# Optimization experiments

Measured on AMD Instinct MI355X. Metric: run time of the kernel, lower is better.

Reference implementation:

```python
import jax, jax.numpy as jnp
import numpy as np

NUM_HEADS = 8  # init num_heads


def setup_inputs() -> dict:
    key = jax.random.key(0)
    ks = jax.random.split(key, 8)
    B, N, C, G = 2, 256 * 256, 256, 512  # N hardcoded by original reshape(256*256)
    xq = jax.random.normal(ks[0], (B, N, C), jnp.float32)
    xk = jax.random.normal(ks[1], (B, N, C), jnp.float32)
    xv = jax.random.normal(ks[2], (B, N, C), jnp.float32)
    w_scale = C ** -0.5
    Wq = jax.random.normal(ks[3], (C, C), jnp.float32) * w_scale
    bq = jax.random.normal(ks[4], (C,), jnp.float32) * 0.02
    Wp = jax.random.normal(ks[5], (C, C), jnp.float32) * w_scale
    bp = jax.random.normal(ks[6], (C,), jnp.float32) * 0.02
    # Voronoi cell labels 1..G, each cell exactly N//G tokens, randomly scattered
    # over the 256x256 grid (irregular gather/scatter access, all cells < 1500 tokens).
    labels = jnp.repeat(jnp.arange(1, G + 1, dtype=jnp.int32), N // G)
    Voronoi = jnp.stack([
        jax.random.permutation(jax.random.fold_in(ks[7], b), labels) for b in range(B)
    ]).reshape(B, 256, 256)
    return {"xq": xq, "xk": xk, "xv": xv, "Wq": Wq, "bq": bq,
            "Wp": Wp, "bp": bp, "Voronoi": Voronoi, "num_groups": G}


def reference(xq, xk, xv, Wq, bq, Wp, bp, Voronoi, num_groups):
    B, N, C = xq.shape
    H = NUM_HEADS
    hd = C // H
    scale = hd ** -0.5  # qk_scale default: head_dim ** -0.5
    # NOTE: the original forward projects q, k AND v with self.q (shared weights/bias).
    # This (likely a bug upstream) is preserved faithfully here.
    q = (xq @ Wq.T + bq).reshape(B, N, H, hd)
    k = (xk @ Wq.T + bq).reshape(B, N, H, hd)
    v = (xv @ Wq.T + bq).reshape(B, N, H, hd)
    labels = Voronoi.reshape(B, N)
    order = jnp.argsort(labels, axis=1)   # [B, N] sort tokens by Voronoi cell id
    inv = jnp.argsort(order, axis=1)      # inverse permutation for scatter-back
    S = N // num_groups                   # tokens per cell (static)

    def gather(t):  # [B, N, H, hd] -> [B, G, S, H, hd] grouped by cell
        return jnp.take_along_axis(t, order[:, :, None, None], axis=1).reshape(B, num_groups, S, H, hd)

    qg = gather(q) * scale
    kg = gather(k)
    vg = gather(v)
    attn = jnp.einsum('bgshd,bgthd->bghst', qg, kg)   # per-cell scores [B,G,H,S,S]
    p = jax.nn.softmax(attn, axis=-1)                 # attn_drop=0 (eval)
    og = jnp.einsum('bghst,bgthd->bgshd', p, vg).reshape(B, N, H, hd)
    out = jnp.take_along_axis(og, inv[:, :, None, None], axis=1).reshape(B, N, C)
    return out @ Wp.T + bp                            # proj_drop=0 (eval)
```

## Files before the change

### kernel.cpp

```cpp
#include <hip/hip_runtime.h>
#include <hip/hip_bf16.h>

#define B_    2
#define NTOK  65536
#define C_    256
#define H_    8
#define HD_   32
#define G_    512
#define S_    128
#define BN    (B_*NTOK)
#define M3    (3*BN)

typedef __attribute__((ext_vector_type(8))) short short8;
typedef __attribute__((ext_vector_type(4))) float f32x4;

__device__ __forceinline__ ushort f2bf(float f) {
  __bf16 h = (__bf16)f;
  return __builtin_bit_cast(unsigned short, h);
}
__device__ __forceinline__ unsigned pk2(float lo, float hi) {
  return (unsigned)f2bf(lo) | ((unsigned)f2bf(hi) << 16);
}

__device__ __forceinline__ void gl16(const void* g, void* l) {
  __builtin_amdgcn_global_load_lds(
      (const __attribute__((address_space(1))) unsigned int*)g,
      (__attribute__((address_space(3))) unsigned int*)l, 16, 0, 0);
}

#define SW4(c, r) ((((c) ^ (r) ^ ((r) >> 2))) & 3)
#define SWK32(c, r) ((((c) ^ ((r) >> 1))) & 3)
#define VSL(c, ch) ((((c) ^ (((ch) & 7) << 1) ^ (((ch) >> 3) & 3))) & 15)

#define QSCALE 0.25506907131737264f

__global__ __launch_bounds__(256) void k_prep(const float* __restrict__ Wq,
                                              const float* __restrict__ Wp,
                                              ushort* __restrict__ Wq_img,
                                              ushort* __restrict__ Wp_img) {
  int gid = blockIdx.x * 256 + threadIdx.x;
  int w = gid >> 13, rem = gid & 8191;
  if (w == 0) {
    int ks = rem >> 11, rem2 = rem & 2047;
    int r = rem2 >> 3, c = rem2 & 7;
    const float4* s = reinterpret_cast<const float4*>(Wq + (size_t)r * 256 + ks * 64 + c * 8);
    float4 a = s[0], b = s[1];
    uint4 o;
    o.x = pk2(a.x, a.y); o.y = pk2(a.z, a.w);
    o.z = pk2(b.x, b.y); o.w = pk2(b.z, b.w);
    *reinterpret_cast<uint4*>(Wq_img + ks * 16384 + r * 64 + ((c ^ (r & 7)) << 3)) = o;
  } else {
    int h = rem >> 10, r = (rem >> 2) & 255, c = rem & 3;
    const float4* s = reinterpret_cast<const float4*>(Wp + (size_t)r * 256 + h * 32 + c * 8);
    float4 a = s[0], b = s[1];
    uint4 o;
    o.x = pk2(a.x, a.y); o.y = pk2(a.z, a.w);
    o.z = pk2(b.x, b.y); o.w = pk2(b.z, b.w);
    *reinterpret_cast<uint4*>(Wp_img + h * 8192 + r * 32 + (SWK32(c, r) << 3)) = o;
  }
}

__global__ __launch_bounds__(256) void k_group(const int* __restrict__ vor,
                                               int* __restrict__ grp,
                                               int* __restrict__ cnt) {
  int idx = blockIdx.x * 256 + threadIdx.x;
  int b = idx >> 16;
  int n = idx & (NTOK - 1);
  int g = vor[idx] - 1;
  int pos = atomicAdd(&cnt[(b << 9) + g], 1);
  grp[((b << 9) + g) * S_ + pos] = n;
}

__global__ __launch_bounds__(512, 4) void k_proj_qkv(
    const float* __restrict__ xq, const float* __restrict__ xk,
    const float* __restrict__ xv, const ushort* __restrict__ Wq_img,
    const float* __restrict__ bq, ushort* __restrict__ qkv) {
  __shared__ ushort As[128 * 64];
  __shared__ ushort Bs[2][256 * 64];
  int mt = blockIdx.x;
  int t = mt >> 10;
  const float* A = (t == 0) ? xq : (t == 1) ? xk : xv;
  float qsc = (t == 0) ? QSCALE : 1.0f;
  size_t abase = (size_t)(mt & 1023) * 128 * 256;
  int row0 = mt * 128;

  int tid = threadIdx.x, lane = tid & 63, wave = tid >> 6;
  int l15 = lane & 15, hi = lane >> 4;
  int wr = (wave >> 2) * 64, wc = (wave & 3) * 64;
  int sr = tid >> 2, sq = tid & 3;

  const float* aptr = A + abase + (size_t)sr * 256 + sq * 16;
  int boff = wave * 4096 + lane * 16;

  f32x4 acc[4][4] = {};
  float4 ar[2][4];
  {
    const float4* p = reinterpret_cast<const float4*>(aptr);
#pragma unroll
    for (int j = 0; j < 4; ++j) ar[0][j] = p[j];
  }
#pragma unroll
  for (int j = 0; j < 4; ++j)
    gl16((const char*)Wq_img + boff + j * 1024, (char*)Bs[0] + boff + j * 1024);

#pragma unroll
  for (int ks = 0; ks < 4; ++ks) {
    uint4 w0, w1;
    w0.x = pk2(ar[ks & 1][0].x, ar[ks & 1][0].y); w0.y = pk2(ar[ks & 1][0].z, ar[ks & 1][0].w);
    w0.z = pk2(ar[ks & 1][1].x, ar[ks & 1][1].y); w0.w = pk2(ar[ks & 1][1].z, ar[ks & 1][1].w);
    w1.x = pk2(ar[ks & 1][2].x, ar[ks & 1][2].y); w1.y = pk2(ar[ks & 1][2].z, ar[ks & 1][2].w);
    w1.z = pk2(ar[ks & 1][3].x, ar[ks & 1][3].y); w1.w = pk2(ar[ks & 1][3].z, ar[ks & 1][3].w);
    *reinterpret_cast<uint4*>(&As[sr * 64 + (((sq * 2) ^ (sr & 7)) << 3)]) = w0;
    *reinterpret_cast<uint4*>(&As[sr * 64 + (((sq * 2 + 1) ^ (sr & 7)) << 3)]) = w1;
    if (ks < 3) {
      const float4* p = reinterpret_cast<const float4*>(aptr + (ks + 1) * 64);
#pragma unroll
      for (int j = 0; j < 4; ++j) ar[(ks + 1) & 1][j] = p[j];
#pragma unroll
      for (int j = 0; j < 4; ++j)
        gl16((const char*)Wq_img + (ks + 1) * 32768 + boff + j * 1024,
             (char*)Bs[(ks + 1) & 1] + boff + j * 1024);
      asm volatile("s_waitcnt vmcnt(8)" ::: "memory");
    } else {
      asm volatile("s_waitcnt vmcnt(0)" ::: "memory");
    }
    asm volatile("s_waitcnt lgkmcnt(0)" ::: "memory");
    __builtin_amdgcn_s_barrier();
    const ushort* Bcur = Bs[ks & 1];
#pragma unroll
    for (int kk = 0; kk < 2; ++kk) {
      int ck = kk * 4 + hi;
      short8 af[4], bfr[4];
#pragma unroll
      for (int m = 0; m < 4; ++m) {
        int r = wr + m * 16 + l15;
        af[m] = *reinterpret_cast<const short8*>(&As[r * 64 + ((ck ^ (r & 7)) << 3)]);
      }
#pragma unroll
      for (int n = 0; n < 4; ++n) {
        int r = wc + n * 16 + l15;
        bfr[n] = *reinterpret_cast<const short8*>(&Bcur[r * 64 + ((ck ^ (r & 7)) << 3)]);
      }
#pragma unroll
      for (int m = 0; m < 4; ++m)
#pragma unroll
        for (int n = 0; n < 4; ++n)
          acc[m][n] = __builtin_amdgcn_mfma_f32_16x16x32_bf16(af[m], bfr[n], acc[m][n], 0, 0, 0);
    }
    asm volatile("s_waitcnt lgkmcnt(0)" ::: "memory");
    __builtin_amdgcn_s_barrier();
  }

  ushort* Ot = (ushort*)Bs;
#pragma unroll
  for (int n = 0; n < 4; ++n) {
    int col = wc + n * 16 + l15;
    float bv = bq[col];
    int c = col >> 3, ci = col & 7;
#pragma unroll
    for (int m = 0; m < 4; ++m) {
      int r0 = wr + m * 16 + hi * 4;
#pragma unroll
      for (int j = 0; j < 4; ++j) {
        int r = r0 + j;
        int slot = c ^ (((r >> 2) & 3) << 1);
        Ot[r * 256 + slot * 8 + ci] = f2bf((acc[m][n][j] + bv) * qsc);
      }
    }
  }
  __syncthreads();
  {
    size_t gbase = (size_t)row0 * 256;
#pragma unroll
    for (int s = 0; s < 8; ++s) {
      int off = s * 4096 + tid * 8;
      int r = off >> 8, cc = (off >> 3) & 31;
      int slot = cc ^ (((r >> 2) & 3) << 1);
      *reinterpret_cast<uint4*>(qkv + gbase + off) =
          *reinterpret_cast<const uint4*>(Ot + r * 256 + slot * 8);
    }
  }
}

__global__ __launch_bounds__(512) void k_attn_proj(
    const ushort* __restrict__ qkv, const int* __restrict__ grp,
    const ushort* __restrict__ Wp_img, const float* __restrict__ bp,
    float* __restrict__ out) {
  __shared__ int toks[128];
  __shared__ ushort shm[32768];
  ushort* Qs  = shm;
  ushort* Ks  = shm + 4096;
  ushort* Vt  = shm + 8192;
  ushort* Oh  = shm + 12288;
  ushort* Wp0 = shm + 16384;
  ushort* Wp1 = shm + 24576;

  int bid = blockIdx.x;
  int g = bid & (G_ - 1), b = bid >> 9;
  int tid = threadIdx.x, lane = tid & 63, wave = tid >> 6;
  int l15 = lane & 15, hi = lane >> 4;
  int strip = wave * 16;
  int mg = wave >> 1, ng = wave & 1;

  if (tid < 128) toks[tid] = grp[((b << 9) + g) * S_ + tid];
  __syncthreads();

  int wpoff = wave * 1024 + lane * 16;
  gl16((const char*)Wp_img + wpoff, (char*)Wp0 + wpoff);
  gl16((const char*)Wp_img + 8192 + wpoff, (char*)Wp0 + wpoff + 8192);

  f32x4 acc[2][8] = {};

  int r_st = tid >> 2, cp = tid & 3;
  int tok_st = toks[r_st];
  size_t rowq = (size_t)(b * NTOK + tok_st) * 256;
  int chunk_t = r_st >> 3, tl = r_st & 7;

  uint4 qa, ka, va;
  {
    size_t base = rowq + cp * 8;
    qa = *reinterpret_cast<const uint4*>(qkv + base);
    ka = *reinterpret_cast<const uint4*>(qkv + (size_t)BN * 256 + base);
    va = *reinterpret_cast<const uint4*>(qkv + (size_t)2 * BN * 256 + base);
  }

  for (int h = 0; h < 8; ++h) {
    ushort* WpCur = (h & 1) ? Wp1 : Wp0;
    ushort* WpNext = (h & 1) ? Wp0 : Wp1;
    *reinterpret_cast<uint4*>(&Qs[r_st * 32 + SW4(cp, r_st) * 8]) = qa;
    *reinterpret_cast<uint4*>(&Ks[r_st * 32 + SW4(cp, r_st) * 8]) = ka;
    {
      const ushort* pv_ = reinterpret_cast<const ushort*>(&va);
#pragma unroll
      for (int e = 0; e < 8; ++e) {
        int ch = cp * 8 + e;
        Vt[ch * 128 + (VSL(chunk_t, ch) << 3) + tl] = pv_[e];
      }
    }
    asm volatile("s_waitcnt lgkmcnt(0)" ::: "memory");
    __builtin_amdgcn_s_barrier();

    if (h < 7) {
      gl16((const char*)Wp_img + (h + 1) * 16384 + wpoff, (char*)WpNext + wpoff);
      gl16((const char*)Wp_img + (h + 1) * 16384 + 8192 + wpoff, (char*)WpNext + wpoff + 8192);
      size_t base = rowq + (h + 1) * 32 + cp * 8;
      qa = *reinterpret_cast<const uint4*>(qkv + base);
      ka = *reinterpret_cast<const uint4*>(qkv + (size_t)BN * 256 + base);
      va = *reinterpret_cast<const uint4*>(qkv + (size_t)2 * BN * 256 + base);
    }

    f32x4 sacc[8] = {};
    {
      int ra = strip + l15;
      short8 qf = *reinterpret_cast<const short8*>(&Qs[ra * 32 + SW4(hi, ra) * 8]);
      __builtin_amdgcn_s_setprio(1);
#pragma unroll
      for (int n = 0; n < 8; ++n) {
        int r = n * 16 + l15;
        short8 kf = *reinterpret_cast<const short8*>(&Ks[r * 32 + SW4(hi, r) * 8]);
        sacc[n] = __builtin_amdgcn_mfma_f32_16x16x32_bf16(kf, qf, sacc[n], 0, 0, 0);
      }
      __builtin_amdgcn_s_setprio(0);
    }

    float mx = -1e30f;
#pragma unroll
    for (int n = 0; n < 8; ++n)
#pragma unroll
      for (int j = 0; j < 4; ++j) mx = fmaxf(mx, sacc[n][j]);
    mx = fmaxf(mx, __shfl_xor(mx, 16));
    mx = fmaxf(mx, __shfl_xor(mx, 32));
    float p[8][4];
    float sum = 0.f;
#pragma unroll
    for (int n = 0; n < 8; ++n)
#pragma unroll
      for (int j = 0; j < 4; ++j) { p[n][j] = exp2f(sacc[n][j] - mx); sum += p[n][j]; }
    sum += __shfl_xor(sum, 16);
    sum += __shfl_xor(sum, 32);
    float inv = 1.0f / sum;

    short8 paf[4];
#pragma unroll
    for (int t = 0; t < 4; ++t) {
      unsigned e0 = pk2(p[2 * t][0], p[2 * t][1]);
      unsigned e1 = pk2(p[2 * t][2], p[2 * t][3]);
      unsigned o0 = pk2(p[2 * t + 1][0], p[2 * t + 1][1]);
      unsigned o1 = pk2(p[2 * t + 1][2], p[2 * t + 1][3]);
      unsigned pe0 = __shfl_xor(e0, 16), pe1 = __shfl_xor(e1, 16);
      unsigned po0 = __shfl_xor(o0, 16), po1 = __shfl_xor(o1, 16);
      bool up = (hi & 1);
      unsigned E0 = up ? pe0 : e0, E1 = up ? pe1 : e1;
      unsigned E2 = up ? e0 : pe0, E3 = up ? e1 : pe1;
      unsigned O0 = up ? po0 : o0, O1 = up ? po1 : o1;
      unsigned O2 = up ? o0 : po0, O3 = up ? o1 : po1;
      unsigned s0 = up ? E0 : O0, s1 = up ? E1 : O1;
      unsigned s2 = up ? E2 : O2, s3 = up ? E3 : O3;
      unsigned r0 = __shfl_xor(s0, 32), r1 = __shfl_xor(s1, 32);
      unsigned r2 = __shfl_xor(s2, 32), r3 = __shfl_xor(s3, 32);
      unsigned f0, f1, f2, f3;
      if (hi == 0)      { f0 = E0; f1 = E1; f2 = E2; f3 = E3; }
      else if (hi == 3) { f0 = O0; f1 = O1; f2 = O2; f3 = O3; }
      else              { f0 = r0; f1 = r1; f2 = r2; f3 = r3; }
      union { unsigned u[4]; short8 s; } cv;
      cv.u[0] = f0; cv.u[1] = f1; cv.u[2] = f2; cv.u[3] = f3;
      paf[t] = cv.s;
    }

    f32x4 oacc[2] = {};
    __builtin_amdgcn_s_setprio(1);
#pragma unroll
    for (int t = 0; t < 4; ++t) {
      short8 bv[2];
#pragma unroll
      for (int n2 = 0; n2 < 2; ++n2) {
        int ch = n2 * 16 + l15;
        int chunk = t * 4 + hi;
        bv[n2] = *reinterpret_cast<const short8*>(&Vt[ch * 128 + (VSL(chunk, ch) << 3)]);
      }
#pragma unroll
      for (int n2 = 0; n2 < 2; ++n2)
        oacc[n2] = __builtin_amdgcn_mfma_f32_16x16x32_bf16(paf[t], bv[n2], oacc[n2], 0, 0, 0);
    }
    __builtin_amdgcn_s_setprio(0);

    float invj[4];
#pragma unroll
    for (int jr = 0; jr < 4; ++jr) invj[jr] = __shfl(inv, hi * 4 + jr);
#pragma unroll
    for (int n2 = 0; n2 < 2; ++n2)
#pragma unroll
      for (int jr = 0; jr < 4; ++jr) {
        int row = strip + hi * 4 + jr;
        int col = n2 * 16 + l15;
        Oh[row * 32 + (SWK32(col >> 3, row) << 3) + (col & 7)] = f2bf(oacc[n2][jr] * invj[jr]);
      }
    asm volatile("s_waitcnt vmcnt(5)" ::: "memory");
    asm volatile("s_waitcnt lgkmcnt(0)" ::: "memory");
    __builtin_amdgcn_s_barrier();

    {
      short8 af[2], bf[8];
#pragma unroll
      for (int m = 0; m < 2; ++m) {
        int r = mg * 32 + m * 16 + l15;
        af[m] = *reinterpret_cast<const short8*>(&Oh[r * 32 + (SWK32(hi, r) << 3)]);
      }
#pragma unroll
      for (int n = 0; n < 8; ++n) {
        int r = ng * 128 + n * 16 + l15;
        bf[n] = *reinterpret_cast<const short8*>(&WpCur[r * 32 + (SWK32(hi, r) << 3)]);
      }
      __builtin_amdgcn_s_setprio(1);
#pragma unroll
      for (int m = 0; m < 2; ++m)
#pragma unroll
        for (int n = 0; n < 8; ++n)
          acc[m][n] = __builtin_amdgcn_mfma_f32_16x16x32_bf16(af[m], bf[n], acc[m][n], 0, 0, 0);
      __builtin_amdgcn_s_setprio(0);
    }
  }

  float* Of = (float*)shm;
#pragma unroll
  for (int q = 0; q < 4; ++q) {
    __syncthreads();
    if (mg == q) {
#pragma unroll
      for (int n = 0; n < 8; ++n) {
        int col = ng * 128 + n * 16 + l15;
        float bv = bp[col];
        int c = col >> 2, ci = col & 3;
#pragma unroll
        for (int m = 0; m < 2; ++m) {
#pragma unroll
          for (int j = 0; j < 4; ++j) {
            int lr = m * 16 + hi * 4 + j;
            int slot = c ^ (((lr >> 2) & 3) << 2);
            Of[lr * 256 + slot * 4 + ci] = acc[m][n][j] + bv;
          }
        }
      }
    }
    __syncthreads();
#pragma unroll
    for (int s = 0; s < 4; ++s) {
      int off = s * 2048 + tid * 4;
      int lr = off >> 8, cc = (off >> 2) & 63;
      int slot = cc ^ (((lr >> 2) & 3) << 2);
      int tok = toks[q * 32 + lr];
      *reinterpret_cast<float4*>(out + ((size_t)(b * NTOK + tok)) * 256 + cc * 4) =
          *reinterpret_cast<const float4*>(Of + lr * 256 + slot * 4);
    }
  }
}

extern "C" void kernel_launch(void* const* d_in, const int* in_sizes, int n_in,
                              void* d_out, int out_size, void* d_ws, size_t ws_size,
                              hipStream_t stream) {
  const float* xq = (const float*)d_in[0];
  const float* xk = (const float*)d_in[1];
  const float* xv = (const float*)d_in[2];
  const float* Wq = (const float*)d_in[3];
  const float* bq = (const float*)d_in[4];
  const float* Wp = (const float*)d_in[5];
  const float* bp = (const float*)d_in[6];
  const int*   vor = (const int*)d_in[7];

  char* ws = (char*)d_ws;
  ushort* qkv    = (ushort*)ws;
  int*    grp    = (int*)(ws + (size_t)201326592);
  int*    cnt    = (int*)(ws + (size_t)201850880);
  ushort* Wq_img = (ushort*)(ws + (size_t)201854976);
  ushort* Wp_img = (ushort*)(ws + (size_t)201986048);

  hipMemsetAsync(cnt, 0, B_ * G_ * sizeof(int), stream);
  k_prep<<<dim3(64), dim3(256), 0, stream>>>(Wq, Wp, Wq_img, Wp_img);
  k_group<<<dim3(BN / 256), dim3(256), 0, stream>>>(vor, grp, cnt);
  k_proj_qkv<<<dim3(M3 / 128), dim3(512), 0, stream>>>(xq, xk, xv, Wq_img, bq, qkv);
  k_attn_proj<<<dim3(B_ * G_), dim3(512), 0, stream>>>(qkv, grp, Wp_img, bp, (float*)d_out);
}
```

Measured before the change: 316.0 us.

## Make QKV projection persistent with full weight matrix resident in LDS

The QKV projection becomes a persistent kernel with 256 blocks. Each block loads the whole bf16 Wq image (128KB) into LDS once, and each wave then walks independent 32-row tiles over six iterations, with no block-level barriers inside the main loop. The goal is to stop re-streaming the weights per 128-row tile and to cut barrier overhead, with per-wave staging for A and for the output transpose. In exchange, the large LDS footprint limits occupancy to one block per CU, each wave does less MFMA work per A fragment (2x16 tiles), and latency hiding relies on register double-buffering of A.

```diff
diff --git a/kernel.cpp b/kernel.cpp
--- a/kernel.cpp
+++ b/kernel.cpp
@@ -41,14 +41,13 @@
   int gid = blockIdx.x * 256 + threadIdx.x;
   int w = gid >> 13, rem = gid & 8191;
   if (w == 0) {
-    int ks = rem >> 11, rem2 = rem & 2047;
-    int r = rem2 >> 3, c = rem2 & 7;
-    const float4* s = reinterpret_cast<const float4*>(Wq + (size_t)r * 256 + ks * 64 + c * 8);
+    int ks = rem >> 10, r = (rem >> 2) & 255, c = rem & 3;
+    const float4* s = reinterpret_cast<const float4*>(Wq + (size_t)r * 256 + ks * 32 + c * 8);
     float4 a = s[0], b = s[1];
     uint4 o;
     o.x = pk2(a.x, a.y); o.y = pk2(a.z, a.w);
     o.z = pk2(b.x, b.y); o.w = pk2(b.z, b.w);
-    *reinterpret_cast<uint4*>(Wq_img + ks * 16384 + r * 64 + ((c ^ (r & 7)) << 3)) = o;
+    *reinterpret_cast<uint4*>(Wq_img + ks * 8192 + r * 32 + (SWK32(c, r) << 3)) = o;
   } else {
     int h = rem >> 10, r = (rem >> 2) & 255, c = rem & 3;
     const float4* s = reinterpret_cast<const float4*>(Wp + (size_t)r * 256 + h * 32 + c * 8);
@@ -71,113 +70,113 @@
   grp[((b << 9) + g) * S_ + pos] = n;
 }
 
-__global__ __launch_bounds__(512, 4) void k_proj_qkv(
+__global__ __launch_bounds__(512, 2) void k_proj_qkv(
     const float* __restrict__ xq, const float* __restrict__ xk,
     const float* __restrict__ xv, const ushort* __restrict__ Wq_img,
     const float* __restrict__ bq, ushort* __restrict__ qkv) {
-  __shared__ ushort As[128 * 64];
-  __shared__ ushort Bs[2][256 * 64];
-  int mt = blockIdx.x;
-  int t = mt >> 10;
-  const float* A = (t == 0) ? xq : (t == 1) ? xk : xv;
-  float qsc = (t == 0) ? QSCALE : 1.0f;
-  size_t abase = (size_t)(mt & 1023) * 128 * 256;
-  int row0 = mt * 128;
-
+  __shared__ ushort Wl[65536];
+  __shared__ ushort Asl[8][1024];
   int tid = threadIdx.x, lane = tid & 63, wave = tid >> 6;
   int l15 = lane & 15, hi = lane >> 4;
-  int wr = (wave >> 2) * 64, wc = (wave & 3) * 64;
-  int sr = tid >> 2, sq = tid & 3;
-
-  const float* aptr = A + abase + (size_t)sr * 256 + sq * 16;
-  int boff = wave * 4096 + lane * 16;
-
-  f32x4 acc[4][4] = {};
+
+  {
+    int off = tid * 16;
+#pragma unroll
+    for (int s = 0; s < 16; ++s)
+      gl16((const char*)Wq_img + s * 8192 + off, (char*)Wl + s * 8192 + off);
+  }
+  asm volatile("s_waitcnt vmcnt(0)" ::: "memory");
+  __syncthreads();
+
+  ushort* As = Asl[wave];
+  int sr = lane >> 1, sc2 = (lane & 1) * 2;
+
+  float biasv[16];
+#pragma unroll
+  for (int n = 0; n < 16; ++n) biasv[n] = bq[n * 16 + l15];
+
+  int gw = blockIdx.x * 8 + wave;
+
   float4 ar[2][4];
   {
-    const float4* p = reinterpret_cast<const float4*>(aptr);
-#pragma unroll
-    for (int j = 0; j < 4; ++j) ar[0][j] = p[j];
-  }
-#pragma unroll
-  for (int j = 0; j < 4; ++j)
-    gl16((const char*)Wq_img + boff + j * 1024, (char*)Bs[0] + boff + j * 1024);
-
-#pragma unroll
-  for (int ks = 0; ks < 4; ++ks) {
-    uint4 w0, w1;
-    w0.x = pk2(ar[ks & 1][0].x, ar[ks & 1][0].y); w0.y = pk2(ar[ks & 1][0].z, ar[ks & 1][0].w);
-    w0.z = pk2(ar[ks & 1][1].x, ar[ks & 1][1].y); w0.w = pk2(ar[ks & 1][1].z, ar[ks & 1][1].w);
-    w1.x = pk2(ar[ks & 1][2].x, ar[ks & 1][2].y); w1.y = pk2(ar[ks & 1][2].z, ar[ks & 1][2].w);
-    w1.z = pk2(ar[ks & 1][3].x, ar[ks & 1][3].y); w1.w = pk2(ar[ks & 1][3].z, ar[ks & 1][3].w);
-    *reinterpret_cast<uint4*>(&As[sr * 64 + (((sq * 2) ^ (sr & 7)) << 3)]) = w0;
-    *reinterpret_cast<uint4*>(&As[sr * 64 + (((sq * 2 + 1) ^ (sr & 7)) << 3)]) = w1;
-    if (ks < 3) {
-      const float4* p = reinterpret_cast<const float4*>(aptr + (ks + 1) * 64);
-#pragma unroll
-      for (int j = 0; j < 4; ++j) ar[(ks + 1) & 1][j] = p[j];
-#pragma unroll
-      for (int j = 0; j < 4; ++j)
-        gl16((const char*)Wq_img + (ks + 1) * 32768 + boff + j * 1024,
-             (char*)Bs[(ks + 1) & 1] + boff + j * 1024);
-      asm volatile("s_waitcnt vmcnt(8)" ::: "memory");
-    } else {
-      asm volatile("s_waitcnt vmcnt(0)" ::: "memory");
-    }
-    asm volatile("s_waitcnt lgkmcnt(0)" ::: "memory");
-    __builtin_amdgcn_s_barrier();
-    const ushort* Bcur = Bs[ks & 1];
-#pragma unroll
-    for (int kk = 0; kk < 2; ++kk) {
-      int ck = kk * 4 + hi;
-      short8 af[4], bfr[4];
-#pragma unroll
-      for (int m = 0; m < 4; ++m) {
-        int r = wr + m * 16 + l15;
-        af[m] = *reinterpret_cast<const short8*>(&As[r * 64 + ((ck ^ (r & 7)) << 3)]);
-      }
-#pragma unroll
-      for (int n = 0; n < 4; ++n) {
-        int r = wc + n * 16 + l15;
-        bfr[n] = *reinterpret_cast<const short8*>(&Bcur[r * 64 + ((ck ^ (r & 7)) << 3)]);
-      }
-#pragma unroll
-      for (int m = 0; m < 4; ++m)
-#pragma unroll
-        for (int n = 0; n < 4; ++n)
-          acc[m][n] = __builtin_amdgcn_mfma_f32_16x16x32_bf16(af[m], bfr[n], acc[m][n], 0, 0, 0);
-    }
-    asm volatile("s_waitcnt lgkmcnt(0)" ::: "memory");
-    __builtin_amdgcn_s_barrier();
-  }
-
-  ushort* Ot = (ushort*)Bs;
-#pragma unroll
-  for (int n = 0; n < 4; ++n) {
-    int col = wc + n * 16 + l15;
-    float bv = bq[col];
-    int c = col >> 3, ci = col & 7;
-#pragma unroll
-    for (int m = 0; m < 4; ++m) {
-      int r0 = wr + m * 16 + hi * 4;
+    int p = gw;
+    const float* A = (p >> 12) == 0 ? xq : ((p >> 12) == 1 ? xk : xv);
+    const float* aptr = A + (size_t)(p & 4095) * 32 * 256 + (size_t)sr * 256 + (lane & 1) * 16;
+    const float4* p4 = reinterpret_cast<const float4*>(aptr);
+#pragma unroll
+    for (int j = 0; j < 4; ++j) ar[0][j] = p4[j];
+  }
+
+  for (int it = 0; it < 6; ++it) {
+    int p = gw + it * 2048;
+    int t = p >> 12;
+    const float* A = (t == 0) ? xq : (t == 1) ? xk : xv;
+    float qsc = (t == 0) ? QSCALE : 1.0f;
+    const float* aptr = A + (size_t)(p & 4095) * 32 * 256 + (size_t)sr * 256 + (lane & 1) * 16;
+
+    f32x4 acc[2][16] = {};
+
+#pragma unroll
+    for (int ks = 0; ks < 8; ++ks) {
+      {
+        uint4 w0, w1;
+        w0.x = pk2(ar[ks & 1][0].x, ar[ks & 1][0].y); w0.y = pk2(ar[ks & 1][0].z, ar[ks & 1][0].w);
+        w0.z = pk2(ar[ks & 1][1].x, ar[ks & 1][1].y); w0.w = pk2(ar[ks & 1][1].z, ar[ks & 1][1].w);
+        w1.x = pk2(ar[ks & 1][2].x, ar[ks & 1][2].y); w1.y = pk2(ar[ks & 1][2].z, ar[ks & 1][2].w);
+        w1.z = pk2(ar[ks & 1][3].x, ar[ks & 1][3].y); w1.w = pk2(ar[ks & 1][3].z, ar[ks & 1][3].w);
+        *reinterpret_cast<uint4*>(&As[sr * 32 + (SWK32(sc2, sr) << 3)]) = w0;
+        *reinterpret_cast<uint4*>(&As[sr * 32 + (SWK32(sc2 + 1, sr) << 3)]) = w1;
+      }
+      if (ks < 7) {
+        const float4* p4 = reinterpret_cast<const float4*>(aptr + (ks + 1) * 32);
+#pragma unroll
+        for (int j = 0; j < 4; ++j) ar[(ks + 1) & 1][j] = p4[j];
+      } else if (it < 5) {
+        int pN = gw + (it + 1) * 2048;
+        const float* AN = (pN >> 12) == 0 ? xq : ((pN >> 12) == 1 ? xk : xv);
+        const float* aptrN = AN + (size_t)(pN & 4095) * 32 * 256 + (size_t)sr * 256 + (lane & 1) * 16;
+        const float4* p4 = reinterpret_cast<const float4*>(aptrN);
+#pragma unroll
+        for (int j = 0; j < 4; ++j) ar[0][j] = p4[j];
+      }
+      {
+        short8 af[2];
+#pragma unroll
+        for (int m = 0; m < 2; ++m) {
+          int r = m * 16 + l15;
+          af[m] = *reinterpret_cast<const short8*>(&As[r * 32 + (SWK32(hi, r) << 3)]);
+        }
+#pragma unroll
+        for (int n = 0; n < 16; ++n) {
+          int r = n * 16 + l15;
+          short8 bf = *reinterpret_cast<const short8*>(&Wl[ks * 8192 + r * 32 + (SWK32(hi, r) << 3)]);
+#pragma unroll
+          for (int m = 0; m < 2; ++m)
+            acc[m][n] = __builtin_amdgcn_mfma_f32_16x16x32_bf16(af[m], bf, acc[m][n], 0, 0, 0);
+        }
+      }
+    }
+
+    int row0o = p * 32;
+#pragma unroll
+    for (int m = 0; m < 2; ++m) {
 #pragma unroll
       for (int j = 0; j < 4; ++j) {
-        int r = r0 + j;
-        int slot = c ^ (((r >> 2) & 3) << 1);
-        Ot[r * 256 + slot * 8 + ci] = f2bf((acc[m][n][j] + bv) * qsc);
-      }
-    }
-  }
-  __syncthreads();
-  {
-    size_t gbase = (size_t)row0 * 256;
-#pragma unroll
-    for (int s = 0; s < 8; ++s) {
-      int off = s * 4096 + tid * 8;
-      int r = off >> 8, cc = (off >> 3) & 31;
-      int slot = cc ^ (((r >> 2) & 3) << 1);
-      *reinterpret_cast<uint4*>(qkv + gbase + off) =
-          *reinterpret_cast<const uint4*>(Ot + r * 256 + slot * 8);
+#pragma unroll
+        for (int n = 0; n < 16; ++n)
+          As[hi * 256 + ((n ^ hi) << 4) + l15] = f2bf((acc[m][n][j] + biasv[n]) * qsc);
+#pragma unroll
+        for (int s = 0; s < 2; ++s) {
+          int boff = lane * 16 + s * 1024;
+          int rl = boff >> 9;
+          int cc = (boff >> 5) & 15;
+          int slot = cc ^ rl;
+          uint4 v = *reinterpret_cast<const uint4*>(
+              (const char*)As + rl * 512 + slot * 32 + (boff & 16));
+          int grow = row0o + m * 16 + rl * 4 + j;
+          *reinterpret_cast<uint4*>(qkv + (size_t)grow * 256 + cc * 16 + ((boff & 16) >> 1)) = v;
+        }
+      }
     }
   }
 }
@@ -417,6 +416,6 @@
   hipMemsetAsync(cnt, 0, B_ * G_ * sizeof(int), stream);
   k_prep<<<dim3(64), dim3(256), 0, stream>>>(Wq, Wp, Wq_img, Wp_img);
   k_group<<<dim3(BN / 256), dim3(256), 0, stream>>>(vor, grp, cnt);
-  k_proj_qkv<<<dim3(M3 / 128), dim3(512), 0, stream>>>(xq, xk, xv, Wq_img, bq, qkv);
+  k_proj_qkv<<<dim3(256), dim3(512), 0, stream>>>(xq, xk, xv, Wq_img, bq, qkv);
   k_attn_proj<<<dim3(B_ * G_), dim3(512), 0, stream>>>(qkv, grp, Wp_img, bp, (float*)d_out);
 }
```

Result: slower. 324.7 us (+2.8%).
